# Optimization experiments

Measured on AMD Instinct MI355X. Metric: run time of the kernel, lower is better.

## Reference

```python
import jax, jax.numpy as jnp
import numpy as np

N_NODES = 100000
IN_CH = 2048
OUT_CH = 128
ITERATIONS = 4
NNZ_FEAT = 2000000
NNZ_ADJ = 1600000


def setup_inputs() -> dict:
    key = jax.random.key(0)
    ks = jax.random.split(key, 8)
    feat_rows = jax.random.randint(ks[0], (NNZ_FEAT,), 0, N_NODES, dtype=jnp.int64 if jax.config.jax_enable_x64 else jnp.int32)
    feat_cols = jax.random.randint(ks[1], (NNZ_FEAT,), 0, IN_CH, dtype=feat_rows.dtype)
    feat_values = jax.random.uniform(ks[2], (NNZ_FEAT,), dtype=jnp.float32)
    adj_rows = jax.random.randint(ks[3], (NNZ_ADJ,), 0, N_NODES, dtype=feat_rows.dtype)
    adj_cols = jax.random.randint(ks[4], (NNZ_ADJ,), 0, N_NODES, dtype=feat_rows.dtype)
    # normalized adjacency values ~ 1/degree scale
    adj_values = jax.random.uniform(ks[5], (NNZ_ADJ,), dtype=jnp.float32) * (1.0 / 16.0)
    # xavier_uniform for weight [in, out] and bias [1, out]
    wb = float(np.sqrt(6.0 / (IN_CH + OUT_CH)))
    weight = jax.random.uniform(ks[6], (IN_CH, OUT_CH), minval=-wb, maxval=wb, dtype=jnp.float32)
    bb = float(np.sqrt(6.0 / (1 + OUT_CH)))
    bias = jax.random.uniform(ks[7], (1, OUT_CH), minval=-bb, maxval=bb, dtype=jnp.float32)
    return {
        "feat_rows": feat_rows, "feat_cols": feat_cols, "feat_values": feat_values,
        "adj_rows": adj_rows, "adj_cols": adj_cols, "adj_values": adj_values,
        "weight": weight, "bias": bias,
    }


def _spmm(rows, cols, values, dense, n_out_rows):
    # COO sparse [n_out_rows, *] @ dense [*, d] -> [n_out_rows, d]
    contrib = values[:, None] * dense[cols]  # [nnz, d]
    return jax.ops.segment_sum(contrib, rows, num_segments=n_out_rows)


def reference(feat_rows, feat_cols, feat_values, adj_rows, adj_cols, adj_values, weight, bias):
    # base = spmm(sparse_features, W) + b ; dropout is identity in eval mode
    h = _spmm(feat_rows, feat_cols, feat_values, weight, N_NODES)  # [N, out]
    h = jax.nn.relu(h + bias)
    for _ in range(ITERATIONS - 1):
        h = _spmm(adj_rows, adj_cols, adj_values, h, N_NODES)
    return h
```

## Files before the change

kernel.cpp:

```cpp
#include <hip/hip_runtime.h>
#include <hip/hip_fp16.h>

#define N_NODES 100000
#define IN_CH 2048
#define OUT_CH 128
#define NNZ_FEAT 2000000
#define NNZ_ADJ 1600000
#define NNZ_TOT (NNZ_FEAT + NNZ_ADJ)
#define BROWS 512
#define NBUCK 391
#define NROWP (NBUCK * BROWS)
#define KB_BLOCK 256
#define KB_ITEMS 16
#define KB_CHUNK (KB_BLOCK * KB_ITEMS)
#define KB_GRID ((NNZ_TOT + KB_CHUNK - 1) / KB_CHUNK)

#define PK_COL_BITS 17
#define PK_COL_MASK ((1 << PK_COL_BITS) - 1)


__global__ __launch_bounds__(KB_BLOCK) void kA(const int* __restrict__ frows,
                                               const int* __restrict__ arows,
                                               int* __restrict__ bcnt) {
    __shared__ int hist[NBUCK];
    for (int t = threadIdx.x; t < NBUCK; t += KB_BLOCK) hist[t] = 0;
    __syncthreads();
    long base = (long)blockIdx.x * KB_CHUNK;
    for (int j = 0; j < KB_ITEMS; ++j) {
        long i = base + j * KB_BLOCK + threadIdx.x;
        if (i < NNZ_TOT) {
            int r = (i < NNZ_FEAT) ? frows[i] : (N_NODES + arows[i - NNZ_FEAT]);
            atomicAdd(&hist[r >> 9], 1);
        }
    }
    __syncthreads();
    for (int t = threadIdx.x; t < NBUCK; t += KB_BLOCK)
        if (hist[t]) atomicAdd(&bcnt[t], hist[t]);
}

__global__ void k_scanb(const int* __restrict__ bcnt, int* __restrict__ boff,
                        int* __restrict__ gcur) {
    __shared__ int s[512];
    int t = threadIdx.x;
    int v = (t < NBUCK) ? bcnt[t] : 0;
    s[t] = v;
    __syncthreads();
    for (int off = 1; off < 512; off <<= 1) {
        int x = (t >= off) ? s[t - off] : 0;
        __syncthreads();
        s[t] += x;
        __syncthreads();
    }
    int e = s[t] - v;
    if (t < NBUCK) { boff[t] = e; gcur[t] = e; }
    if (t == NBUCK - 1) boff[NBUCK] = s[t];
}


__global__ __launch_bounds__(KB_BLOCK) void kB(const int* __restrict__ frows,
                                               const int* __restrict__ fcols,
                                               const float* __restrict__ fvals,
                                               const int* __restrict__ arows,
                                               const int* __restrict__ acols,
                                               const float* __restrict__ avals,
                                               int* __restrict__ gcur,
                                               int* __restrict__ tmp_pk,
                                               float* __restrict__ tmp_vl) {
    __shared__ int hist[NBUCK];
    __shared__ int lcnt[NBUCK];
    __shared__ int gb[NBUCK];
    __shared__ int bstart[NBUCK];
    __shared__ int sc[512];
    __shared__ int s_pk[KB_CHUNK];
    __shared__ float s_vl[KB_CHUNK];
    __shared__ unsigned short s_bid[KB_CHUNK];

    int tid = threadIdx.x;
    for (int t = tid; t < NBUCK; t += KB_BLOCK) { hist[t] = 0; lcnt[t] = 0; }
    __syncthreads();

    long base = (long)blockIdx.x * KB_CHUNK;
    int rr[KB_ITEMS];
    for (int j = 0; j < KB_ITEMS; ++j) {
        long i = base + j * KB_BLOCK + tid;
        int r = -1;
        if (i < NNZ_TOT) {
            r = (i < NNZ_FEAT) ? frows[i] : (N_NODES + arows[i - NNZ_FEAT]);
            atomicAdd(&hist[r >> 9], 1);
        }
        rr[j] = r;
    }
    __syncthreads();

    sc[tid] = (tid < NBUCK) ? hist[tid] : 0;
    sc[tid + 256] = (tid + 256 < NBUCK) ? hist[tid + 256] : 0;
    __syncthreads();
    for (int o = 1; o < 512; o <<= 1) {
        int a0 = (tid >= o) ? sc[tid - o] : 0;
        int a1 = ((tid + 256) >= o) ? sc[tid + 256 - o] : 0;
        __syncthreads();
        sc[tid] += a0;
        sc[tid + 256] += a1;
        __syncthreads();
    }
    for (int t = tid; t < NBUCK; t += KB_BLOCK) {
        int h = hist[t];
        bstart[t] = sc[t] - h;
        gb[t] = h ? atomicAdd(&gcur[t], h) : 0;
    }
    __syncthreads();
    int tot = sc[NBUCK - 1];

    for (int j = 0; j < KB_ITEMS; ++j) {
        int r = rr[j];
        if (r >= 0) {
            long i = base + j * KB_BLOCK + tid;
            int c; float v;
            if (i < NNZ_FEAT) { c = fcols[i]; v = fvals[i]; }
            else              { c = acols[i - NNZ_FEAT]; v = avals[i - NNZ_FEAT]; }
            int b = r >> 9;
            int slot = bstart[b] + atomicAdd(&lcnt[b], 1);
            s_pk[slot] = ((r & 511) << PK_COL_BITS) | c;
            s_vl[slot] = v;
            s_bid[slot] = (unsigned short)b;
        }
    }
    __syncthreads();

    for (int s = tid; s < tot; s += KB_BLOCK) {
        int b = s_bid[s];
        int dest = gb[b] + (s - bstart[b]);
        tmp_pk[dest] = s_pk[s];
        tmp_vl[dest] = s_vl[s];
    }
}


__global__ __launch_bounds__(256) void kC1(const int* __restrict__ boff,
                                           const int* __restrict__ tmp_pk,
                                           int* __restrict__ C) {
    __shared__ int rcnt[BROWS];
    int b = blockIdx.x, rbase = b << 9;
    rcnt[threadIdx.x] = 0;
    rcnt[threadIdx.x + 256] = 0;
    __syncthreads();
    int e0 = boff[b], e1 = boff[b + 1];
    for (int i = e0 + threadIdx.x; i < e1; i += 256)
        atomicAdd(&rcnt[tmp_pk[i] >> PK_COL_BITS], 1);
    __syncthreads();
    C[rbase + threadIdx.x] = rcnt[threadIdx.x];
    C[rbase + threadIdx.x + 256] = rcnt[threadIdx.x + 256];
}


__global__ void k_scan1(const int* __restrict__ in, int* __restrict__ out,
                        int* __restrict__ bsums) {
    __shared__ int s[1024];
    int tid = threadIdx.x;
    int i = blockIdx.x * 1024 + tid;
    int v = (i < NROWP) ? in[i] : 0;
    s[tid] = v;
    __syncthreads();
    for (int off = 1; off < 1024; off <<= 1) {
        int t = (tid >= off) ? s[tid - off] : 0;
        __syncthreads();
        s[tid] += t;
        __syncthreads();
    }
    if (i < NROWP) out[i] = s[tid] - v;
    if (tid == 1023) bsums[blockIdx.x] = s[1023];
}

__global__ void k_scan2(int* __restrict__ bsums, int nb) {
    __shared__ int s[256];
    int tid = threadIdx.x;
    int v = (tid < nb) ? bsums[tid] : 0;
    s[tid] = v;
    __syncthreads();
    for (int off = 1; off < 256; off <<= 1) {
        int t = (tid >= off) ? s[tid - off] : 0;
        __syncthreads();
        s[tid] += t;
        __syncthreads();
    }
    if (tid < nb) bsums[tid] = s[tid] - v;
}

__global__ void k_scan3(int* __restrict__ S, const int* __restrict__ bsums) {
    int i = blockIdx.x * 1024 + threadIdx.x;
    if (i < NROWP) S[i] += bsums[blockIdx.x];
}


__global__ __launch_bounds__(256) void kC2(const int* __restrict__ boff,
                                           const int* __restrict__ S,
                                           const int* __restrict__ tmp_pk,
                                           const float* __restrict__ tmp_vl,
                                           int2* __restrict__ pairs) {
    __shared__ int rcur[BROWS];
    int b = blockIdx.x, rbase = b << 9;
    rcur[threadIdx.x] = S[rbase + threadIdx.x];
    rcur[threadIdx.x + 256] = S[rbase + threadIdx.x + 256];
    __syncthreads();
    int e0 = boff[b], e1 = boff[b + 1];
    for (int i = e0 + threadIdx.x; i < e1; i += 256) {
        int pk = tmp_pk[i];
        float v = tmp_vl[i];
        int p = atomicAdd(&rcur[pk >> PK_COL_BITS], 1);
        pairs[p] = make_int2(pk & PK_COL_MASK, __float_as_int(v));
    }
}


__global__ __launch_bounds__(256) void k_wconv(const float* __restrict__ W,
                                               __half2* __restrict__ Wh) {
    int i = blockIdx.x * 256 + threadIdx.x;
    if (i < IN_CH * OUT_CH / 2) {
        float2 f = ((const float2*)W)[i];
        Wh[i] = __floats2half2_rn(f.x, f.y);
    }
}


#define SPMM_BODY(HSRC, ACC_INIT)                                              \
    int row = blockIdx.x * 4 + (threadIdx.x >> 6);                             \
    int lane = threadIdx.x & 63;                                               \
    int k0 = __builtin_amdgcn_readfirstlane(SROW0);                            \
    int k1 = __builtin_amdgcn_readfirstlane(SROW1);                            \
    float2 a0 = ACC_INIT;                                                      \
    float2 a1 = make_float2(0.0f, 0.0f);                                       \
    for (int base = k0; base < k1; base += 64) {                               \
        int idx = base + lane;                                                 \
        int2 pp = (idx < k1) ? pairs[idx] : make_int2(0, 0);                   \
        int n = k1 - base; if (n > 64) n = 64;                                 \
        int full = n & ~7;                                                     \
        for (int jj = 0; jj < full; jj += 8) {                                 \
            _Pragma("unroll")                                                  \
            for (int j = 0; j < 8; ++j) {                                      \
                int c = __builtin_amdgcn_readlane(pp.x, jj + j);               \
                float v = __int_as_float(__builtin_amdgcn_readlane(pp.y, jj + j)); \
                float2 f = __half22float2(HSRC[(size_t)c * (OUT_CH / 2) + lane]); \
                if (j & 1) { a1.x = fmaf(v, f.x, a1.x); a1.y = fmaf(v, f.y, a1.y); } \
                else       { a0.x = fmaf(v, f.x, a0.x); a0.y = fmaf(v, f.y, a0.y); } \
            }                                                                  \
        }                                                                      \
        if (full < n) {                                                        \
            _Pragma("unroll")                                                  \
            for (int j = 0; j < 8; ++j) {                                      \
                int c = __builtin_amdgcn_readlane(pp.x, full + j);             \
                float v = __int_as_float(__builtin_amdgcn_readlane(pp.y, full + j)); \
                float2 f = __half22float2(HSRC[(size_t)c * (OUT_CH / 2) + lane]); \
                if (j & 1) { a1.x = fmaf(v, f.x, a1.x); a1.y = fmaf(v, f.y, a1.y); } \
                else       { a0.x = fmaf(v, f.x, a0.x); a0.y = fmaf(v, f.y, a0.y); } \
            }                                                                  \
        }                                                                      \
    }

__global__ __launch_bounds__(256) void spmm_w(const int* __restrict__ S,
                                              const int2* __restrict__ pairs,
                                              const __half2* __restrict__ Wh,
                                              const float* __restrict__ bias,
                                              __half2* __restrict__ out16) {
#define SROW0 S[row]
#define SROW1 S[row + 1]
    SPMM_BODY(Wh, ((const float2*)bias)[lane])
#undef SROW0
#undef SROW1
    float rx = fmaxf(a0.x + a1.x, 0.0f);
    float ry = fmaxf(a0.y + a1.y, 0.0f);
    out16[(size_t)row * (OUT_CH / 2) + lane] = __floats2half2_rn(rx, ry);
}

__global__ __launch_bounds__(256) void spmm_adj_hh(const int* __restrict__ S,
                                                   const int2* __restrict__ pairs,
                                                   const __half2* __restrict__ hin,
                                                   __half2* __restrict__ hout) {
#define SROW0 S[N_NODES + row]
#define SROW1 S[N_NODES + row + 1]
    SPMM_BODY(hin, make_float2(0.0f, 0.0f))
#undef SROW0
#undef SROW1
    hout[(size_t)row * (OUT_CH / 2) + lane] = __floats2half2_rn(a0.x + a1.x, a0.y + a1.y);
}

__global__ __launch_bounds__(256) void spmm_adj_hf(const int* __restrict__ S,
                                                   const int2* __restrict__ pairs,
                                                   const __half2* __restrict__ hin,
                                                   float* __restrict__ out) {
#define SROW0 S[N_NODES + row]
#define SROW1 S[N_NODES + row + 1]
    SPMM_BODY(hin, make_float2(0.0f, 0.0f))
#undef SROW0
#undef SROW1
    float2 acc;
    acc.x = a0.x + a1.x;
    acc.y = a0.y + a1.y;
    ((float2*)(out + (size_t)row * OUT_CH))[lane] = acc;
}


extern "C" void kernel_launch(void* const* d_in, const int* in_sizes, int n_in,
                              void* d_out, int out_size, void* d_ws, size_t ws_size,
                              hipStream_t stream) {
    const int*   frows = (const int*)d_in[0];
    const int*   fcols = (const int*)d_in[1];
    const float* fvals = (const float*)d_in[2];
    const int*   arows = (const int*)d_in[3];
    const int*   acols = (const int*)d_in[4];
    const float* avals = (const float*)d_in[5];
    const float* W     = (const float*)d_in[6];
    const float* bias  = (const float*)d_in[7];
    float* out = (float*)d_out;

    char* ws = (char*)d_ws;
    size_t off = 0;
    auto alloc = [&](size_t bytes) {
        size_t o = off;
        off = (off + bytes + 255) & ~(size_t)255;
        return o;
    };
    int*  C     = (int*) (ws + alloc((size_t)NROWP * 4));
    int*  S     = (int*) (ws + alloc((size_t)NROWP * 4));
    int*  bcnt  = (int*) (ws + alloc(400 * 4));
    int*  boff  = (int*) (ws + alloc(400 * 4));
    int*  gcur  = (int*) (ws + alloc(400 * 4));
    int*  bsum  = (int*) (ws + alloc(256 * 4));
    int2* pairs = (int2*)(ws + alloc((size_t)NNZ_TOT * 8));
    __half2* Wh = (__half2*)(ws + alloc((size_t)IN_CH * OUT_CH * 2));
    char* hraw  = ws + alloc(2 * (size_t)N_NODES * OUT_CH * 2);
    __half2* hA = (__half2*)hraw;
    __half2* hB = (__half2*)(hraw + (size_t)N_NODES * OUT_CH * 2);
    int*   tmp_pk = (int*)hraw;
    float* tmp_vl = (float*)(hraw + (((size_t)NNZ_TOT * 4 + 255) & ~(size_t)255));
    (void)ws_size; (void)off; (void)in_sizes; (void)n_in; (void)out_size;

    const int nscan = (NROWP + 1023) / 1024;

    hipMemsetAsync(bcnt, 0, 400 * 4, stream);
    k_wconv<<<(IN_CH * OUT_CH / 2 + 255) / 256, 256, 0, stream>>>(W, Wh);
    kA<<<KB_GRID, KB_BLOCK, 0, stream>>>(frows, arows, bcnt);
    k_scanb<<<1, 512, 0, stream>>>(bcnt, boff, gcur);
    kB<<<KB_GRID, KB_BLOCK, 0, stream>>>(frows, fcols, fvals, arows, acols, avals,
                                         gcur, tmp_pk, tmp_vl);
    kC1<<<NBUCK, 256, 0, stream>>>(boff, tmp_pk, C);
    k_scan1<<<nscan, 1024, 0, stream>>>(C, S, bsum);
    k_scan2<<<1, 256, 0, stream>>>(bsum, nscan);
    k_scan3<<<nscan, 1024, 0, stream>>>(S, bsum);
    kC2<<<NBUCK, 256, 0, stream>>>(boff, S, tmp_pk, tmp_vl, pairs);

    spmm_w<<<N_NODES / 4, 256, 0, stream>>>(S, pairs, Wh, bias, hA);

    spmm_adj_hh<<<N_NODES / 4, 256, 0, stream>>>(S, pairs, hA, hB);
    spmm_adj_hh<<<N_NODES / 4, 256, 0, stream>>>(S, pairs, hB, hA);
    spmm_adj_hf<<<N_NODES / 4, 256, 0, stream>>>(S, pairs, hA, out);
}
```

Before: 335.4 us.

## Fuse CSR build into one kernel and split adjacency SpMM by channel halves per XCD

The per-bucket row count, the global scan and the scatter kernels are merged into one kernel. It does an in-block exclusive scan seeded with the bucket offset, which removes four launches and the C/bsum buffers. The adjacency SpMM kernels now launch twice as many blocks. Each wave handles 64 of the 128 channels (one half each), and block IDs are mapped so that XCDs 0-3 and 4-7 each cover one channel half, aiming to halve the working set of h per XCD L2. The cost is that the pairs/index stream is read twice and each lane does scalar half loads instead of half2.

```diff
diff --git a/kernel.cpp b/kernel.cpp
--- a/kernel.cpp
+++ b/kernel.cpp
@@ -136,74 +136,42 @@
 }
 
 
-__global__ __launch_bounds__(256) void kC1(const int* __restrict__ boff,
-                                           const int* __restrict__ tmp_pk,
-                                           int* __restrict__ C) {
+__global__ __launch_bounds__(256) void kC(const int* __restrict__ boff,
+                                          const int* __restrict__ tmp_pk,
+                                          const float* __restrict__ tmp_vl,
+                                          int2* __restrict__ pairs,
+                                          int* __restrict__ S) {
     __shared__ int rcnt[BROWS];
+    __shared__ int sc2[BROWS];
+    __shared__ int rcur[BROWS];
+    int tid = threadIdx.x;
     int b = blockIdx.x, rbase = b << 9;
-    rcnt[threadIdx.x] = 0;
-    rcnt[threadIdx.x + 256] = 0;
+    rcnt[tid] = 0;
+    rcnt[tid + 256] = 0;
     __syncthreads();
     int e0 = boff[b], e1 = boff[b + 1];
-    for (int i = e0 + threadIdx.x; i < e1; i += 256)
+    for (int i = e0 + tid; i < e1; i += 256)
         atomicAdd(&rcnt[tmp_pk[i] >> PK_COL_BITS], 1);
     __syncthreads();
-    C[rbase + threadIdx.x] = rcnt[threadIdx.x];
-    C[rbase + threadIdx.x + 256] = rcnt[threadIdx.x + 256];
-}
-
-
-__global__ void k_scan1(const int* __restrict__ in, int* __restrict__ out,
-                        int* __restrict__ bsums) {
-    __shared__ int s[1024];
-    int tid = threadIdx.x;
-    int i = blockIdx.x * 1024 + tid;
-    int v = (i < NROWP) ? in[i] : 0;
-    s[tid] = v;
-    __syncthreads();
-    for (int off = 1; off < 1024; off <<= 1) {
-        int t = (tid >= off) ? s[tid - off] : 0;
-        __syncthreads();
-        s[tid] += t;
-        __syncthreads();
-    }
-    if (i < NROWP) out[i] = s[tid] - v;
-    if (tid == 1023) bsums[blockIdx.x] = s[1023];
-}
-
-__global__ void k_scan2(int* __restrict__ bsums, int nb) {
-    __shared__ int s[256];
-    int tid = threadIdx.x;
-    int v = (tid < nb) ? bsums[tid] : 0;
-    s[tid] = v;
-    __syncthreads();
-    for (int off = 1; off < 256; off <<= 1) {
-        int t = (tid >= off) ? s[tid - off] : 0;
-        __syncthreads();
-        s[tid] += t;
-        __syncthreads();
-    }
-    if (tid < nb) bsums[tid] = s[tid] - v;
-}
-
-__global__ void k_scan3(int* __restrict__ S, const int* __restrict__ bsums) {
-    int i = blockIdx.x * 1024 + threadIdx.x;
-    if (i < NROWP) S[i] += bsums[blockIdx.x];
-}
-
-
-__global__ __launch_bounds__(256) void kC2(const int* __restrict__ boff,
-                                           const int* __restrict__ S,
-                                           const int* __restrict__ tmp_pk,
-                                           const float* __restrict__ tmp_vl,
-                                           int2* __restrict__ pairs) {
-    __shared__ int rcur[BROWS];
-    int b = blockIdx.x, rbase = b << 9;
-    rcur[threadIdx.x] = S[rbase + threadIdx.x];
-    rcur[threadIdx.x + 256] = S[rbase + threadIdx.x + 256];
-    __syncthreads();
-    int e0 = boff[b], e1 = boff[b + 1];
-    for (int i = e0 + threadIdx.x; i < e1; i += 256) {
+    sc2[tid] = rcnt[tid];
+    sc2[tid + 256] = rcnt[tid + 256];
+    __syncthreads();
+    for (int o = 1; o < 512; o <<= 1) {
+        int a0 = (tid >= o) ? sc2[tid - o] : 0;
+        int a1 = ((tid + 256) >= o) ? sc2[tid + 256 - o] : 0;
+        __syncthreads();
+        sc2[tid] += a0;
+        sc2[tid + 256] += a1;
+        __syncthreads();
+    }
+    int ex0 = e0 + sc2[tid] - rcnt[tid];
+    int ex1 = e0 + sc2[tid + 256] - rcnt[tid + 256];
+    S[rbase + tid] = ex0;
+    S[rbase + tid + 256] = ex1;
+    rcur[tid] = ex0;
+    rcur[tid + 256] = ex1;
+    __syncthreads();
+    for (int i = e0 + tid; i < e1; i += 256) {
         int pk = tmp_pk[i];
         float v = tmp_vl[i];
         int p = atomicAdd(&rcur[pk >> PK_COL_BITS], 1);
@@ -222,80 +190,102 @@
 }
 
 
-#define SPMM_BODY(HSRC, ACC_INIT)                                              \
-    int row = blockIdx.x * 4 + (threadIdx.x >> 6);                             \
-    int lane = threadIdx.x & 63;                                               \
-    int k0 = __builtin_amdgcn_readfirstlane(SROW0);                            \
-    int k1 = __builtin_amdgcn_readfirstlane(SROW1);                            \
-    float2 a0 = ACC_INIT;                                                      \
-    float2 a1 = make_float2(0.0f, 0.0f);                                       \
-    for (int base = k0; base < k1; base += 64) {                               \
-        int idx = base + lane;                                                 \
-        int2 pp = (idx < k1) ? pairs[idx] : make_int2(0, 0);                   \
-        int n = k1 - base; if (n > 64) n = 64;                                 \
-        int full = n & ~7;                                                     \
-        for (int jj = 0; jj < full; jj += 8) {                                 \
-            _Pragma("unroll")                                                  \
-            for (int j = 0; j < 8; ++j) {                                      \
-                int c = __builtin_amdgcn_readlane(pp.x, jj + j);               \
-                float v = __int_as_float(__builtin_amdgcn_readlane(pp.y, jj + j)); \
-                float2 f = __half22float2(HSRC[(size_t)c * (OUT_CH / 2) + lane]); \
-                if (j & 1) { a1.x = fmaf(v, f.x, a1.x); a1.y = fmaf(v, f.y, a1.y); } \
-                else       { a0.x = fmaf(v, f.x, a0.x); a0.y = fmaf(v, f.y, a0.y); } \
-            }                                                                  \
-        }                                                                      \
-        if (full < n) {                                                        \
-            _Pragma("unroll")                                                  \
-            for (int j = 0; j < 8; ++j) {                                      \
-                int c = __builtin_amdgcn_readlane(pp.x, full + j);             \
-                float v = __int_as_float(__builtin_amdgcn_readlane(pp.y, full + j)); \
-                float2 f = __half22float2(HSRC[(size_t)c * (OUT_CH / 2) + lane]); \
-                if (j & 1) { a1.x = fmaf(v, f.x, a1.x); a1.y = fmaf(v, f.y, a1.y); } \
-                else       { a0.x = fmaf(v, f.x, a0.x); a0.y = fmaf(v, f.y, a0.y); } \
-            }                                                                  \
-        }                                                                      \
-    }
-
 __global__ __launch_bounds__(256) void spmm_w(const int* __restrict__ S,
                                               const int2* __restrict__ pairs,
                                               const __half2* __restrict__ Wh,
                                               const float* __restrict__ bias,
                                               __half2* __restrict__ out16) {
-#define SROW0 S[row]
-#define SROW1 S[row + 1]
-    SPMM_BODY(Wh, ((const float2*)bias)[lane])
-#undef SROW0
-#undef SROW1
+    int row = blockIdx.x * 4 + (threadIdx.x >> 6);
+    int lane = threadIdx.x & 63;
+    int k0 = __builtin_amdgcn_readfirstlane(S[row]);
+    int k1 = __builtin_amdgcn_readfirstlane(S[row + 1]);
+    float2 a0 = ((const float2*)bias)[lane];
+    float2 a1 = make_float2(0.0f, 0.0f);
+    for (int base = k0; base < k1; base += 64) {
+        int idx = base + lane;
+        int2 pp = (idx < k1) ? pairs[idx] : make_int2(0, 0);
+        int n = k1 - base; if (n > 64) n = 64;
+        int full = n & ~7;
+        for (int jj = 0; jj < full; jj += 8) {
+#pragma unroll
+            for (int j = 0; j < 8; ++j) {
+                int c = __builtin_amdgcn_readlane(pp.x, jj + j);
+                float v = __int_as_float(__builtin_amdgcn_readlane(pp.y, jj + j));
+                float2 f = __half22float2(Wh[(size_t)c * (OUT_CH / 2) + lane]);
+                if (j & 1) { a1.x = fmaf(v, f.x, a1.x); a1.y = fmaf(v, f.y, a1.y); }
+                else       { a0.x = fmaf(v, f.x, a0.x); a0.y = fmaf(v, f.y, a0.y); }
+            }
+        }
+        if (full < n) {
+#pragma unroll
+            for (int j = 0; j < 8; ++j) {
+                int c = __builtin_amdgcn_readlane(pp.x, full + j);
+                float v = __int_as_float(__builtin_amdgcn_readlane(pp.y, full + j));
+                float2 f = __half22float2(Wh[(size_t)c * (OUT_CH / 2) + lane]);
+                if (j & 1) { a1.x = fmaf(v, f.x, a1.x); a1.y = fmaf(v, f.y, a1.y); }
+                else       { a0.x = fmaf(v, f.x, a0.x); a0.y = fmaf(v, f.y, a0.y); }
+            }
+        }
+    }
     float rx = fmaxf(a0.x + a1.x, 0.0f);
     float ry = fmaxf(a0.y + a1.y, 0.0f);
     out16[(size_t)row * (OUT_CH / 2) + lane] = __floats2half2_rn(rx, ry);
 }
 
+
+#define ADJ_BODY(HGET)                                                          \
+    int bid = blockIdx.x;                                                       \
+    int xcd = bid & 7;                                                          \
+    int g = xcd >> 2;                                                           \
+    int rb = (bid >> 3) * 4 + (xcd & 3);                          \
+    int wid = threadIdx.x >> 6;                                                 \
+    int lane = threadIdx.x & 63;                                                \
+    int row = rb * 4 + wid;                                       \
+    int k0 = __builtin_amdgcn_readfirstlane(S[N_NODES + row]);                  \
+    int k1 = __builtin_amdgcn_readfirstlane(S[N_NODES + row + 1]);              \
+    int ch = g * 64 + lane;                                                     \
+    float a0 = 0.0f, a1 = 0.0f;                                                 \
+    for (int base = k0; base < k1; base += 64) {                                \
+        int idx = base + lane;                                                  \
+        int2 pp = (idx < k1) ? pairs[idx] : make_int2(0, 0);                    \
+        int n = k1 - base; if (n > 64) n = 64;                                  \
+        int full = n & ~7;                                                      \
+        for (int jj = 0; jj < full; jj += 8) {                                  \
+            _Pragma("unroll")                                                   \
+            for (int j = 0; j < 8; ++j) {                                       \
+                int c = __builtin_amdgcn_readlane(pp.x, jj + j);                \
+                float v = __int_as_float(__builtin_amdgcn_readlane(pp.y, jj + j)); \
+                float f = HGET(c);                                              \
+                if (j & 1) a1 = fmaf(v, f, a1); else a0 = fmaf(v, f, a0);       \
+            }                                                                   \
+        }                                                                       \
+        if (full < n) {                                                         \
+            _Pragma("unroll")                                                   \
+            for (int j = 0; j < 8; ++j) {                                       \
+                int c = __builtin_amdgcn_readlane(pp.x, full + j);              \
+                float v = __int_as_float(__builtin_amdgcn_readlane(pp.y, full + j)); \
+                float f = HGET(c);                                              \
+                if (j & 1) a1 = fmaf(v, f, a1); else a0 = fmaf(v, f, a0);       \
+            }                                                                   \
+        }                                                                       \
+    }
+
+#define HGET16(c) __half2float(hin[(size_t)(c) * OUT_CH + ch])
+
 __global__ __launch_bounds__(256) void spmm_adj_hh(const int* __restrict__ S,
                                                    const int2* __restrict__ pairs,
-                                                   const __half2* __restrict__ hin,
-                                                   __half2* __restrict__ hout) {
-#define SROW0 S[N_NODES + row]
-#define SROW1 S[N_NODES + row + 1]
-    SPMM_BODY(hin, make_float2(0.0f, 0.0f))
-#undef SROW0
-#undef SROW1
-    hout[(size_t)row * (OUT_CH / 2) + lane] = __floats2half2_rn(a0.x + a1.x, a0.y + a1.y);
+                                                   const __half* __restrict__ hin,
+                                                   __half* __restrict__ hout) {
+    ADJ_BODY(HGET16)
+    hout[(size_t)row * OUT_CH + ch] = __float2half(a0 + a1);
 }
 
 __global__ __launch_bounds__(256) void spmm_adj_hf(const int* __restrict__ S,
                                                    const int2* __restrict__ pairs,
-                                                   const __half2* __restrict__ hin,
+                                                   const __half* __restrict__ hin,
                                                    float* __restrict__ out) {
-#define SROW0 S[N_NODES + row]
-#define SROW1 S[N_NODES + row + 1]
-    SPMM_BODY(hin, make_float2(0.0f, 0.0f))
-#undef SROW0
-#undef SROW1
-    float2 acc;
-    acc.x = a0.x + a1.x;
-    acc.y = a0.y + a1.y;
-    ((float2*)(out + (size_t)row * OUT_CH))[lane] = acc;
+    ADJ_BODY(HGET16)
+    out[(size_t)row * OUT_CH + ch] = a0 + a1;
 }
 
 
@@ -319,22 +309,18 @@
         off = (off + bytes + 255) & ~(size_t)255;
         return o;
     };
-    int*  C     = (int*) (ws + alloc((size_t)NROWP * 4));
     int*  S     = (int*) (ws + alloc((size_t)NROWP * 4));
     int*  bcnt  = (int*) (ws + alloc(400 * 4));
     int*  boff  = (int*) (ws + alloc(400 * 4));
     int*  gcur  = (int*) (ws + alloc(400 * 4));
-    int*  bsum  = (int*) (ws + alloc(256 * 4));
     int2* pairs = (int2*)(ws + alloc((size_t)NNZ_TOT * 8));
     __half2* Wh = (__half2*)(ws + alloc((size_t)IN_CH * OUT_CH * 2));
     char* hraw  = ws + alloc(2 * (size_t)N_NODES * OUT_CH * 2);
-    __half2* hA = (__half2*)hraw;
-    __half2* hB = (__half2*)(hraw + (size_t)N_NODES * OUT_CH * 2);
+    __half* hA = (__half*)hraw;
+    __half* hB = (__half*)(hraw + (size_t)N_NODES * OUT_CH * 2);
     int*   tmp_pk = (int*)hraw;
     float* tmp_vl = (float*)(hraw + (((size_t)NNZ_TOT * 4 + 255) & ~(size_t)255));
     (void)ws_size; (void)off; (void)in_sizes; (void)n_in; (void)out_size;
-
-    const int nscan = (NROWP + 1023) / 1024;
 
     hipMemsetAsync(bcnt, 0, 400 * 4, stream);
     k_wconv<<<(IN_CH * OUT_CH / 2 + 255) / 256, 256, 0, stream>>>(W, Wh);
@@ -342,15 +328,11 @@
     k_scanb<<<1, 512, 0, stream>>>(bcnt, boff, gcur);
     kB<<<KB_GRID, KB_BLOCK, 0, stream>>>(frows, fcols, fvals, arows, acols, avals,
                                          gcur, tmp_pk, tmp_vl);
-    kC1<<<NBUCK, 256, 0, stream>>>(boff, tmp_pk, C);
-    k_scan1<<<nscan, 1024, 0, stream>>>(C, S, bsum);
-    k_scan2<<<1, 256, 0, stream>>>(bsum, nscan);
-    k_scan3<<<nscan, 1024, 0, stream>>>(S, bsum);
-    kC2<<<NBUCK, 256, 0, stream>>>(boff, S, tmp_pk, tmp_vl, pairs);
-
-    spmm_w<<<N_NODES / 4, 256, 0, stream>>>(S, pairs, Wh, bias, hA);
-
-    spmm_adj_hh<<<N_NODES / 4, 256, 0, stream>>>(S, pairs, hA, hB);
-    spmm_adj_hh<<<N_NODES / 4, 256, 0, stream>>>(S, pairs, hB, hA);
-    spmm_adj_hf<<<N_NODES / 4, 256, 0, stream>>>(S, pairs, hA, out);
-}
+    kC<<<NBUCK, 256, 0, stream>>>(boff, tmp_pk, tmp_vl, pairs, S);
+
+    spmm_w<<<N_NODES / 4, 256, 0, stream>>>(S, pairs, Wh, bias, (__half2*)hA);
+
+    spmm_adj_hh<<<50000, 256, 0, stream>>>(S, pairs, hA, hB);
+    spmm_adj_hh<<<50000, 256, 0, stream>>>(S, pairs, hB, hA);
+    spmm_adj_hf<<<50000, 256, 0, stream>>>(S, pairs, hA, out);
+}
```

After: 375.0 us. 11.8% more time.

## Fuse per-bucket row count, scan and scatter into one kernel

Applied to the files above, without the earlier changes.

Merges the row-count kernel, the three-pass global prefix scan and the scatter kernel into one per-bucket kernel. Each bucket derives its row offsets from a local shared-memory scan plus the bucket base offset boff[b], which works because buckets are already contiguous. This drops four kernel launches and the global C/scan traffic. Each block also re-reads tmp_pk, which was already true across the old two kernels.

```diff
diff --git a/kernel.cpp b/kernel.cpp
--- a/kernel.cpp
+++ b/kernel.cpp
@@ -136,74 +136,42 @@
 }
 
 
-__global__ __launch_bounds__(256) void kC1(const int* __restrict__ boff,
-                                           const int* __restrict__ tmp_pk,
-                                           int* __restrict__ C) {
+__global__ __launch_bounds__(256) void kC(const int* __restrict__ boff,
+                                          const int* __restrict__ tmp_pk,
+                                          const float* __restrict__ tmp_vl,
+                                          int2* __restrict__ pairs,
+                                          int* __restrict__ S) {
     __shared__ int rcnt[BROWS];
+    __shared__ int sc2[BROWS];
+    __shared__ int rcur[BROWS];
+    int tid = threadIdx.x;
     int b = blockIdx.x, rbase = b << 9;
-    rcnt[threadIdx.x] = 0;
-    rcnt[threadIdx.x + 256] = 0;
+    rcnt[tid] = 0;
+    rcnt[tid + 256] = 0;
     __syncthreads();
     int e0 = boff[b], e1 = boff[b + 1];
-    for (int i = e0 + threadIdx.x; i < e1; i += 256)
+    for (int i = e0 + tid; i < e1; i += 256)
         atomicAdd(&rcnt[tmp_pk[i] >> PK_COL_BITS], 1);
     __syncthreads();
-    C[rbase + threadIdx.x] = rcnt[threadIdx.x];
-    C[rbase + threadIdx.x + 256] = rcnt[threadIdx.x + 256];
-}
-
-
-__global__ void k_scan1(const int* __restrict__ in, int* __restrict__ out,
-                        int* __restrict__ bsums) {
-    __shared__ int s[1024];
-    int tid = threadIdx.x;
-    int i = blockIdx.x * 1024 + tid;
-    int v = (i < NROWP) ? in[i] : 0;
-    s[tid] = v;
-    __syncthreads();
-    for (int off = 1; off < 1024; off <<= 1) {
-        int t = (tid >= off) ? s[tid - off] : 0;
-        __syncthreads();
-        s[tid] += t;
-        __syncthreads();
-    }
-    if (i < NROWP) out[i] = s[tid] - v;
-    if (tid == 1023) bsums[blockIdx.x] = s[1023];
-}
-
-__global__ void k_scan2(int* __restrict__ bsums, int nb) {
-    __shared__ int s[256];
-    int tid = threadIdx.x;
-    int v = (tid < nb) ? bsums[tid] : 0;
-    s[tid] = v;
-    __syncthreads();
-    for (int off = 1; off < 256; off <<= 1) {
-        int t = (tid >= off) ? s[tid - off] : 0;
-        __syncthreads();
-        s[tid] += t;
-        __syncthreads();
-    }
-    if (tid < nb) bsums[tid] = s[tid] - v;
-}
-
-__global__ void k_scan3(int* __restrict__ S, const int* __restrict__ bsums) {
-    int i = blockIdx.x * 1024 + threadIdx.x;
-    if (i < NROWP) S[i] += bsums[blockIdx.x];
-}
-
-
-__global__ __launch_bounds__(256) void kC2(const int* __restrict__ boff,
-                                           const int* __restrict__ S,
-                                           const int* __restrict__ tmp_pk,
-                                           const float* __restrict__ tmp_vl,
-                                           int2* __restrict__ pairs) {
-    __shared__ int rcur[BROWS];
-    int b = blockIdx.x, rbase = b << 9;
-    rcur[threadIdx.x] = S[rbase + threadIdx.x];
-    rcur[threadIdx.x + 256] = S[rbase + threadIdx.x + 256];
-    __syncthreads();
-    int e0 = boff[b], e1 = boff[b + 1];
-    for (int i = e0 + threadIdx.x; i < e1; i += 256) {
+    sc2[tid] = rcnt[tid];
+    sc2[tid + 256] = rcnt[tid + 256];
+    __syncthreads();
+    for (int o = 1; o < 512; o <<= 1) {
+        int a0 = (tid >= o) ? sc2[tid - o] : 0;
+        int a1 = ((tid + 256) >= o) ? sc2[tid + 256 - o] : 0;
+        __syncthreads();
+        sc2[tid] += a0;
+        sc2[tid + 256] += a1;
+        __syncthreads();
+    }
+    int ex0 = e0 + sc2[tid] - rcnt[tid];
+    int ex1 = e0 + sc2[tid + 256] - rcnt[tid + 256];
+    S[rbase + tid] = ex0;
+    S[rbase + tid + 256] = ex1;
+    rcur[tid] = ex0;
+    rcur[tid + 256] = ex1;
+    __syncthreads();
+    for (int i = e0 + tid; i < e1; i += 256) {
         int pk = tmp_pk[i];
         float v = tmp_vl[i];
         int p = atomicAdd(&rcur[pk >> PK_COL_BITS], 1);
@@ -319,12 +287,10 @@
         off = (off + bytes + 255) & ~(size_t)255;
         return o;
     };
-    int*  C     = (int*) (ws + alloc((size_t)NROWP * 4));
     int*  S     = (int*) (ws + alloc((size_t)NROWP * 4));
     int*  bcnt  = (int*) (ws + alloc(400 * 4));
     int*  boff  = (int*) (ws + alloc(400 * 4));
     int*  gcur  = (int*) (ws + alloc(400 * 4));
-    int*  bsum  = (int*) (ws + alloc(256 * 4));
     int2* pairs = (int2*)(ws + alloc((size_t)NNZ_TOT * 8));
     __half2* Wh = (__half2*)(ws + alloc((size_t)IN_CH * OUT_CH * 2));
     char* hraw  = ws + alloc(2 * (size_t)N_NODES * OUT_CH * 2);
@@ -334,19 +300,13 @@
     float* tmp_vl = (float*)(hraw + (((size_t)NNZ_TOT * 4 + 255) & ~(size_t)255));
     (void)ws_size; (void)off; (void)in_sizes; (void)n_in; (void)out_size;
 
-    const int nscan = (NROWP + 1023) / 1024;
-
     hipMemsetAsync(bcnt, 0, 400 * 4, stream);
     k_wconv<<<(IN_CH * OUT_CH / 2 + 255) / 256, 256, 0, stream>>>(W, Wh);
     kA<<<KB_GRID, KB_BLOCK, 0, stream>>>(frows, arows, bcnt);
     k_scanb<<<1, 512, 0, stream>>>(bcnt, boff, gcur);
     kB<<<KB_GRID, KB_BLOCK, 0, stream>>>(frows, fcols, fvals, arows, acols, avals,
                                          gcur, tmp_pk, tmp_vl);
-    kC1<<<NBUCK, 256, 0, stream>>>(boff, tmp_pk, C);
-    k_scan1<<<nscan, 1024, 0, stream>>>(C, S, bsum);
-    k_scan2<<<1, 256, 0, stream>>>(bsum, nscan);
-    k_scan3<<<nscan, 1024, 0, stream>>>(S, bsum);
-    kC2<<<NBUCK, 256, 0, stream>>>(boff, S, tmp_pk, tmp_vl, pairs);
+    kC<<<NBUCK, 256, 0, stream>>>(boff, tmp_pk, tmp_vl, pairs, S);
 
     spmm_w<<<N_NODES / 4, 256, 0, stream>>>(S, pairs, Wh, bias, hA);
 
```

After: 325.6 us. 2.9% less time.
